# Performance work log

Measured on AMD Instinct MI355X. Metric: run time of the kernel, lower is better.

Reference implementation:

```python
import jax, jax.numpy as jnp
import numpy as np

B, L = 2, 256
CHAR, WORD = 8000, 50000
CE, WE, HID, REL = 128, 128, 256, 24
IN_DIM = CE + WE


def _lstm(x, mask, W, U, b):
    # Keras LSTM cell: z = x@W + h@U + b split into (i,f,g,o); masked steps carry state through.
    # x: (B, T, D) float, mask: (B, T) bool
    h0 = jnp.zeros((x.shape[0], U.shape[0]), x.dtype)

    def step(carry, xm):
        h, c = carry
        xt, mt = xm
        z = xt @ W + h @ U + b
        i, f, g, o = jnp.split(z, 4, axis=-1)
        c_new = jax.nn.sigmoid(f) * c + jax.nn.sigmoid(i) * jnp.tanh(g)
        h_new = jax.nn.sigmoid(o) * jnp.tanh(c_new)
        m = mt[:, None]
        h2 = jnp.where(m, h_new, h)
        c2 = jnp.where(m, c_new, c)
        return (h2, c2), h2

    _, hs = jax.lax.scan(step, (h0, h0), (jnp.swapaxes(x, 0, 1), jnp.swapaxes(mask, 0, 1)))
    return jnp.swapaxes(hs, 0, 1)  # (B, T, HID)


def _head(enc, Wu, bu, Wv, bv, Wuv, buv, Wc, bc):
    # Original: tile relu(u) over axis 1 (depends on j) and relu(v) over axis 2 (depends on i),
    # concat -> Dense. Equivalent fused form: split Wuv and broadcast-add the two projections.
    u = jax.nn.relu(enc @ Wu + bu)  # (B, L, E)
    v = jax.nn.relu(enc @ Wv + bv)  # (B, L, E)
    E = Wu.shape[1]
    uv = (jnp.einsum('bjd,de->bje', u, Wuv[:E])[:, None, :, :]
          + jnp.einsum('bid,de->bie', v, Wuv[E:])[:, :, None, :]
          + buv)  # (B, L, L, E)
    return uv @ Wc + bc  # (B, L, L, out)


def setup_inputs() -> dict:
    key = jax.random.key(0)
    ks = jax.random.split(key, 64)

    def w(k, shape):
        return jax.random.normal(k, shape, jnp.float32) * 0.05

    inp = {
        'inputs': jax.random.randint(ks[0], (B, L), 0, CHAR, jnp.int32),
        'input_words': jax.random.randint(ks[1], (B, L), 0, WORD, jnp.int32),
        'input_max_len': L,
        'embed_table': w(ks[2], (CHAR, CE)),
        'word_embed_table': w(ks[3], (WORD, WE)),
        'lstm_fwd_W': w(ks[4], (IN_DIM, 4 * HID)),
        'lstm_fwd_U': w(ks[5], (HID, 4 * HID)),
        'lstm_fwd_b': jnp.zeros((4 * HID,), jnp.float32),
        'lstm_bwd_W': w(ks[6], (IN_DIM, 4 * HID)),
        'lstm_bwd_U': w(ks[7], (HID, 4 * HID)),
        'lstm_bwd_b': jnp.zeros((4 * HID,), jnp.float32),
    }
    i = 8
    for name, out in (('eh', 1), ('hh', REL), ('tt', REL)):
        inp[f'{name}_u_W'] = w(ks[i], (2 * HID, CE)); i += 1
        inp[f'{name}_u_b'] = jnp.zeros((CE,), jnp.float32)
        inp[f'{name}_v_W'] = w(ks[i], (2 * HID, CE)); i += 1
        inp[f'{name}_v_b'] = jnp.zeros((CE,), jnp.float32)
        inp[f'{name}_uv_W'] = w(ks[i], (2 * CE, CE)); i += 1
        inp[f'{name}_uv_b'] = jnp.zeros((CE,), jnp.float32)
        inp[f'{name}_cls_W'] = w(ks[i], (CE, out)); i += 1
        inp[f'{name}_cls_b'] = jnp.zeros((out,), jnp.float32)
    return inp


def reference(inputs, input_words, input_max_len, embed_table, word_embed_table,
              lstm_fwd_W, lstm_fwd_U, lstm_fwd_b, lstm_bwd_W, lstm_bwd_U, lstm_bwd_b,
              eh_u_W, eh_u_b, eh_v_W, eh_v_b, eh_uv_W, eh_uv_b, eh_cls_W, eh_cls_b,
              hh_u_W, hh_u_b, hh_v_W, hh_v_b, hh_uv_W, hh_uv_b, hh_cls_W, hh_cls_b,
              tt_u_W, tt_u_b, tt_v_W, tt_v_b, tt_uv_W, tt_uv_b, tt_cls_W, tt_cls_b):
    mask = inputs != 0  # (B, L)
    x = jnp.concatenate([embed_table[inputs], word_embed_table[input_words]], axis=-1)
    h_fwd = _lstm(x, mask, lstm_fwd_W, lstm_fwd_U, lstm_fwd_b)
    h_bwd = _lstm(x[:, ::-1], mask[:, ::-1], lstm_bwd_W, lstm_bwd_U, lstm_bwd_b)[:, ::-1]
    enc = jnp.concatenate([h_fwd, h_bwd], axis=-1)  # (B, L, 2*HID)
    eh = jax.nn.sigmoid(_head(enc, eh_u_W, eh_u_b, eh_v_W, eh_v_b, eh_uv_W, eh_uv_b, eh_cls_W, eh_cls_b))
    hh = jax.nn.softmax(_head(enc, hh_u_W, hh_u_b, hh_v_W, hh_v_b, hh_uv_W, hh_uv_b, hh_cls_W, hh_cls_b), axis=-1)
    tt = jax.nn.softmax(_head(enc, tt_u_W, tt_u_b, tt_v_W, tt_v_b, tt_uv_W, tt_uv_b, tt_cls_W, tt_cls_b), axis=-1)
    return (eh, hh, tt)
```

## Files before the change

### kernel.cpp

```cpp
#include <hip/hip_runtime.h>
#include <hip/hip_bf16.h>

typedef unsigned short u16;
typedef unsigned int u32;
typedef unsigned long long u64;

#define LSEQ 256

constexpr int XW_F  = 0;
constexpr int XW_B  = 524288;
constexpr int HF_O  = 1048576;
constexpr int HB_O  = 1179648;
constexpr int UV_O  = 1310720;
constexpr int PEH_O = 1703936;
constexpr int QEH_O = 1704448;
constexpr int PHH_O = 1704960;
constexpr int QHH_O = 1717248;
constexpr int PTT_O = 1729536;
constexpr int QTT_O = 1741824;
constexpr int DT_O  = 1754128;
constexpr int CW_WF = 1754240;
constexpr int CW_UF = 2016384;
constexpr int CW_BF = 2278528;
constexpr int CW_WB = 2279552;
constexpr int CW_UB = 2541696;
constexpr int CW_BB = 2803840;
constexpr int HD0   = 2804864;
constexpr int HDS   = 167424;
constexpr int HD1   = HD0 + HDS;
constexpr int HD2   = HD0 + 2 * HDS;

constexpr u64 SENT64 = 0x7FC000007FC00000ULL;

__device__ __forceinline__ float b2f(u16 u) {
  u32 x = ((u32)u) << 16; float f;
  __builtin_memcpy(&f, &x, 4); return f;
}
__device__ __forceinline__ u16 f2b(float f) {
  u32 x; __builtin_memcpy(&x, &f, 4);
  u32 r = (x + 0x7fffu + ((x >> 16) & 1u)) >> 16;
  return (u16)r;
}
__device__ __forceinline__ float sigm(float x) {
  return __builtin_amdgcn_rcpf(1.f + __expf(-x));
}
__device__ __forceinline__ float tanh_fast(float x) {
  return 2.f * __builtin_amdgcn_rcpf(1.f + __expf(-2.f * x)) - 1.f;
}
__device__ __forceinline__ u64 aload64(u64* p) {
  return __hip_atomic_load(p, __ATOMIC_RELAXED, __HIP_MEMORY_SCOPE_AGENT);
}
__device__ __forceinline__ void astore64(u64* p, u64 v) {
  __hip_atomic_store(p, v, __ATOMIC_RELAXED, __HIP_MEMORY_SCOPE_AGENT);
}

__global__ __launch_bounds__(256) void k_detect(const void* __restrict__ etab,
                                                float* __restrict__ ws)
{
  __shared__ int cnt;
  const int tid = threadIdx.x;
  if (tid == 0) cnt = 0;
  __syncthreads();
  const u32 w = ((const u32*)etab)[tid];
  if (w & 0x4000u) atomicAdd(&cnt, 1);
  __syncthreads();
  if (tid == 0) ws[DT_O] = (cnt >= 16) ? 1.0f : 0.0f;
}

struct PtrPack { const void* p[30]; };

__global__ __launch_bounds__(256) void k_convert(PtrPack pk, float* __restrict__ ws)
{
  const int cnts[30] = {
    262144, 262144, 1024, 262144, 262144, 1024,
    65536, 128, 65536, 128, 32768, 128, 128, 1,
    65536, 128, 65536, 128, 32768, 128, 3072, 24,
    65536, 128, 65536, 128, 32768, 128, 3072, 24};
  const int dsts[30] = {
    CW_WF, CW_UF, CW_BF, CW_WB, CW_UB, CW_BB,
    HD0, HD0 + 65536, HD0 + 65664, HD0 + 131200, HD0 + 131328, HD0 + 164096, HD0 + 164224, HD0 + 167296,
    HD1, HD1 + 65536, HD1 + 65664, HD1 + 131200, HD1 + 131328, HD1 + 164096, HD1 + 164224, HD1 + 167296,
    HD2, HD2 + 65536, HD2 + 65664, HD2 + 131200, HD2 + 131328, HD2 + 164096, HD2 + 164224, HD2 + 167296};
  const int job = blockIdx.y;
  const int n = cnts[job];
  float* dst = ws + dsts[job];
  const void* src = pk.p[job];
  const bool f32m = ws[DT_O] > 0.5f;
  const int tid = threadIdx.x;
  const int idx = blockIdx.x * 256 + tid;
  const int stride = 64 * 256;
  const int n4 = n >> 2;
  if (f32m) {
    const float4* s = (const float4*)src;
    float4* d = (float4*)dst;
    for (int i = idx; i < n4; i += stride) d[i] = s[i];
  } else {
    const ushort4* s = (const ushort4*)src;
    float4* d = (float4*)dst;
    for (int i = idx; i < n4; i += stride) {
      ushort4 v = s[i];
      d[i] = make_float4(b2f(v.x), b2f(v.y), b2f(v.z), b2f(v.w));
    }
  }
  if (blockIdx.x == 0) {
    for (int i = (n4 << 2) + tid; i < n; i += 256)
      dst[i] = f32m ? ((const float*)src)[i] : b2f(((const u16*)src)[i]);
  }
}

__global__ __launch_bounds__(256) void k_embed_xw(
    const int* __restrict__ toks, const int* __restrict__ wrds,
    const void* __restrict__ etab, const void* __restrict__ wtab,
    float* __restrict__ ws)
{
  __shared__ float xs[8][256];
  const int tid = threadIdx.x, blk = blockIdx.x;
  {
    u64* hz = (u64*)(ws + HF_O) + (blk * 256 + tid) * 8;
#pragma unroll
    for (int m = 0; m < 8; m++) astore64(hz + m, SENT64);
  }
  const bool f32m = ws[DT_O] > 0.5f;
  for (int rr = 0; rr < 8; rr++) {
    const int row = blk * 8 + rr;
    const int id = toks[row], wid = wrds[row];
    float v;
    if (f32m) {
      v = (tid < 128) ? ((const float*)etab)[id * 128 + tid]
                      : ((const float*)wtab)[wid * 128 + (tid - 128)];
    } else {
      v = (tid < 128) ? b2f(((const u16*)etab)[id * 128 + tid])
                      : b2f(((const u16*)wtab)[wid * 128 + (tid - 128)]);
    }
    xs[rr][tid] = v;
  }
  __syncthreads();
  float aF[8][4], aB[8][4];
#pragma unroll
  for (int rr = 0; rr < 8; rr++)
#pragma unroll
    for (int c = 0; c < 4; c++) { aF[rr][c] = 0.f; aB[rr][c] = 0.f; }
  const float2* Wf2 = (const float2*)(ws + CW_WF);
  const float2* Wb2 = (const float2*)(ws + CW_WB);
  for (int k = 0; k < 256; k++) {
    const float2 wfa = Wf2[k * 512 + tid];
    const float2 wfb = Wf2[k * 512 + 256 + tid];
    const float2 wba = Wb2[k * 512 + tid];
    const float2 wbb = Wb2[k * 512 + 256 + tid];
#pragma unroll
    for (int rr = 0; rr < 8; rr++) {
      const float x = xs[rr][k];
      aF[rr][0] = fmaf(x, wfa.x, aF[rr][0]); aF[rr][1] = fmaf(x, wfa.y, aF[rr][1]);
      aF[rr][2] = fmaf(x, wfb.x, aF[rr][2]); aF[rr][3] = fmaf(x, wfb.y, aF[rr][3]);
      aB[rr][0] = fmaf(x, wba.x, aB[rr][0]); aB[rr][1] = fmaf(x, wba.y, aB[rr][1]);
      aB[rr][2] = fmaf(x, wbb.x, aB[rr][2]); aB[rr][3] = fmaf(x, wbb.y, aB[rr][3]);
    }
  }
  const int c0 = 2 * tid, c2 = 512 + 2 * tid;
#pragma unroll
  for (int rr = 0; rr < 8; rr++) {
    const int row = blk * 8 + rr;
    float* of = ws + XW_F + row * 1024;
    of[c0]   = aF[rr][0] + ws[CW_BF + c0];
    of[c0+1] = aF[rr][1] + ws[CW_BF + c0 + 1];
    of[c2]   = aF[rr][2] + ws[CW_BF + c2];
    of[c2+1] = aF[rr][3] + ws[CW_BF + c2 + 1];
    float* ob = ws + XW_B + row * 1024;
    ob[c0]   = aB[rr][0] + ws[CW_BB + c0];
    ob[c0+1] = aB[rr][1] + ws[CW_BB + c0 + 1];
    ob[c2]   = aB[rr][2] + ws[CW_BB + c2];
    ob[c2+1] = aB[rr][3] + ws[CW_BB + c2 + 1];
  }
}

__global__ __launch_bounds__(256, 1) void k_lstm(
    const int* __restrict__ toks, float* __restrict__ ws)
{
  __shared__ float2 hsh[2][256];
  __shared__ float psum[8][256];
  __shared__ float zsh[256];
  __shared__ int msk[512];
  const int tid = threadIdx.x;
  const int dir = blockIdx.x >> 3, chunk = blockIdx.x & 7, base = chunk * 32;
  const int q = tid & 31, ksec = tid >> 5, k0 = ksec * 32;
  u64* h64 = (u64*)(ws + (dir ? HB_O : HF_O));
  const float* xw = ws + (dir ? XW_B : XW_F);
  const float* Ubase = ws + (dir ? CW_UB : CW_UF);

  const int lc0 = 4 * q;
  const int gc0 = ((lc0 >> 5) << 8) + base + (lc0 & 31);
  float4 us[32];
#pragma unroll
  for (int j = 0; j < 32; j++)
    us[j] = *(const float4*)(Ubase + (k0 + j) * 1024 + gc0);

  const int gu = tid & 31, bsel = tid >> 5;
  const int rb = tid >> 7, rc = tid & 127;
  const int rgc = ((rc >> 5) << 8) + base + (rc & 31);
  const int widx = tid - 32;
  const int pkk = widx + (widx >= base ? 32 : 0);

  float cReg = 0.f, hReg = 0.f;
  float xwreg = xw[(rb * 256 + (dir ? 255 : 0)) * 1024 + rgc];

  hsh[0][tid] = make_float2(0.f, 0.f);
  msk[tid] = toks[tid];
  msk[tid + 256] = toks[tid + 256];
  __syncthreads();

  for (int s = 0; s < LSEQ; s++) {
    const int par = s & 1, npar = par ^ 1;
    const int t = dir ? (255 - s) : s;
    float a00 = 0.f, a01 = 0.f, a02 = 0.f, a03 = 0.f;
    float a10 = 0.f, a11 = 0.f, a12 = 0.f, a13 = 0.f;
#pragma unroll
    for (int j = 0; j < 32; j++) {
      const float2 h = hsh[par][k0 + j];
      const float4 uu = us[j];
      a00 = fmaf(h.x, uu.x, a00); a01 = fmaf(h.x, uu.y, a01);
      a02 = fmaf(h.x, uu.z, a02); a03 = fmaf(h.x, uu.w, a03);
      a10 = fmaf(h.y, uu.x, a10); a11 = fmaf(h.y, uu.y, a11);
      a12 = fmaf(h.y, uu.z, a12); a13 = fmaf(h.y, uu.w, a13);
    }
    *(float4*)&psum[ksec][lc0]       = make_float4(a00, a01, a02, a03);
    *(float4*)&psum[ksec][128 + lc0] = make_float4(a10, a11, a12, a13);
    __syncthreads();
    {
      float z = xwreg;
#pragma unroll
      for (int ks = 0; ks < 8; ks++) z += psum[ks][rb * 128 + rc];
      zsh[rb * 128 + rc] = z;
    }
    const int t2 = dir ? (s < 255 ? 254 - s : 255) : (s < 255 ? s + 1 : 0);
    xwreg = xw[(rb * 256 + t2) * 1024 + rgc];
    __syncthreads();
    if (tid < 64) {
      const float* zr = &zsh[bsel * 128];
      const float zi = zr[gu], zf = zr[32 + gu], zg = zr[64 + gu], zo = zr[96 + gu];
      const float cn = sigm(zf) * cReg + sigm(zi) * tanh_fast(zg);
      const float hn = sigm(zo) * tanh_fast(cn);
      if (msk[bsel * 256 + t] != 0) { cReg = cn; hReg = hn; }
      const float hb1 = __shfl_xor(hReg, 32);
      if (tid < 32) {
        const float2 fv = make_float2(hReg, hb1);
        hsh[npar][base + gu] = fv;
        u64 pv; __builtin_memcpy(&pv, &fv, 8);
        astore64(h64 + s * 256 + base + gu, pv);
      }
    }
    if (tid >= 32 && s < 255) {
      u64* p = h64 + s * 256 + pkk;
      u64 v = aload64(p);
      while (v == SENT64) v = aload64(p);
      float2 hv; __builtin_memcpy(&hv, &v, 8);
      hsh[npar][pkk] = hv;
    }
    __syncthreads();
  }
}

__global__ __launch_bounds__(256) void k_uv(float* __restrict__ ws)
{
  __shared__ float encs[8][512];
  const int tid = threadIdx.x, blk = blockIdx.x;
  for (int i = tid; i < 4096; i += 256) {
    const int rr = i >> 9, h = i & 511;
    const int row = blk * 8 + rr, b = row >> 8, t = row & 255;
    encs[rr][h] = (h < 256)
        ? ws[HF_O + t * 512 + h * 2 + b]
        : ws[HB_O + (255 - t) * 512 + (h - 256) * 2 + b];
  }
  __syncthreads();
  const float* wp[3]; float bias[3]; int mats[3], cs[3];
#pragma unroll
  for (int g = 0; g < 3; g++) {
    const int colid = tid + (g << 8);
    mats[g] = colid >> 7; cs[g] = colid & 127;
    const int head = mats[g] >> 1, part = mats[g] & 1;
    wp[g]  = ws + HD0 + head * HDS + (part ? 65664 : 0) + cs[g];
    bias[g] = ws[HD0 + head * HDS + (part ? 131200 : 65536) + cs[g]];
  }
  float acc[3][8];
#pragma unroll
  for (int g = 0; g < 3; g++)
#pragma unroll
    for (int rr = 0; rr < 8; rr++) acc[g][rr] = 0.f;
  for (int k = 0; k < 512; k++) {
#pragma unroll
    for (int g = 0; g < 3; g++) {
      const float w = wp[g][k * 128];
#pragma unroll
      for (int rr = 0; rr < 8; rr++)
        acc[g][rr] = fmaf(encs[rr][k], w, acc[g][rr]);
    }
  }
#pragma unroll
  for (int g = 0; g < 3; g++)
#pragma unroll
    for (int rr = 0; rr < 8; rr++) {
      const int row = blk * 8 + rr;
      ws[UV_O + (mats[g] * 512 + row) * 128 + cs[g]] = fmaxf(acc[g][rr] + bias[g], 0.f);
    }
}

__global__ __launch_bounds__(128) void k_pq(float* __restrict__ ws)
{
  __shared__ float us[4][6][128];
  __shared__ float ash[4][3][128], qsh[4][3][128];
  const int blk = blockIdx.x, tid = threadIdx.x;
  for (int i = tid; i < 3072; i += 128) {
    const int rr = i / 768, rem = i % 768, mat = rem >> 7, e = rem & 127;
    us[rr][mat][e] = ws[UV_O + (mat * 512 + blk * 4 + rr) * 128 + e];
  }
  __syncthreads();
#pragma unroll
  for (int hd = 0; hd < 3; hd++) {
    const float* W = ws + HD0 + hd * HDS + 131328;
    float av[4] = {0.f, 0.f, 0.f, 0.f}, qv[4] = {0.f, 0.f, 0.f, 0.f};
    for (int k = 0; k < 128; k++) {
      const float w1 = W[k * 128 + tid];
      const float w2 = W[(128 + k) * 128 + tid];
#pragma unroll
      for (int rr = 0; rr < 4; rr++) {
        av[rr] = fmaf(us[rr][2 * hd][k], w1, av[rr]);
        qv[rr] = fmaf(us[rr][2 * hd + 1][k], w2, qv[rr]);
      }
    }
    const float buv = ws[HD0 + hd * HDS + 164096 + tid];
#pragma unroll
    for (int rr = 0; rr < 4; rr++) {
      ash[rr][hd][tid] = av[rr] + buv;
      qsh[rr][hd][tid] = qv[rr];
    }
  }
  __syncthreads();
  if (tid < 98) {
    for (int rr = 0; rr < 4; rr++) {
      const int row = blk * 4 + rr;
      const float* src; float* dst; const float* Wc; int o, nout;
      if (tid < 2) {
        Wc = ws + HD0 + 164224; nout = 1; o = 0;
        src = (tid == 0) ? ash[rr][0] : qsh[rr][0];
        dst = ws + ((tid == 0) ? PEH_O : QEH_O) + row;
      } else if (tid < 50) {
        Wc = ws + HD1 + 164224; nout = 24;
        if (tid < 26) { o = tid - 2;  src = ash[rr][1]; dst = ws + PHH_O + row * 24 + o; }
        else          { o = tid - 26; src = qsh[rr][1]; dst = ws + QHH_O + row * 24 + o; }
      } else {
        Wc = ws + HD2 + 164224; nout = 24;
        if (tid < 74) { o = tid - 50; src = ash[rr][2]; dst = ws + PTT_O + row * 24 + o; }
        else          { o = tid - 74; src = qsh[rr][2]; dst = ws + QTT_O + row * 24 + o; }
      }
      float acc = 0.f;
      for (int e = 0; e < 128; e++) acc = fmaf(src[e], Wc[e * nout + o], acc);
      *dst = acc;
    }
  }
}

__global__ __launch_bounds__(256) void k_out(const float* __restrict__ ws,
                                             void* __restrict__ outv)
{
  __shared__ float qh[24], qt[24];
  __shared__ float qe_s;
  __shared__ u32 sh[3072], st[3072];
  const bool f32m = ws[DT_O] > 0.5f;
  const int bi = blockIdx.x, b = bi >> 8, i = bi & 255;
  const int j = threadIdx.x;
  if (j < 24)       qh[j] = ws[QHH_O + (b * 256 + i) * 24 + j] + ws[HD1 + 167296 + j];
  else if (j < 48)  qt[j - 24] = ws[QTT_O + (b * 256 + i) * 24 + (j - 24)] + ws[HD2 + 167296 + (j - 24)];
  else if (j == 48) qe_s = ws[QEH_O + b * 256 + i] + ws[HD0 + 167296];
  __syncthreads();
  {
    float v = ws[PEH_O + b * 256 + j] + qe_s;
    v = 1.f / (1.f + __expf(-v));
    if (f32m) ((float*)outv)[(b * 256 + i) * 256 + j] = v;
    else      ((u16*)outv)[(b * 256 + i) * 256 + j] = f2b(v);
  }
  float p[24];
  {
    const float* pp = ws + PHH_O + (b * 256 + j) * 24;
    float mx = -1e30f;
#pragma unroll
    for (int o = 0; o < 24; o++) { p[o] = pp[o] + qh[o]; mx = fmaxf(mx, p[o]); }
    float ssum = 0.f;
#pragma unroll
    for (int o = 0; o < 24; o++) { p[o] = __expf(p[o] - mx); ssum += p[o]; }
    const float inv = 1.f / ssum;
    if (f32m) {
      float* dst = (float*)outv + 131072 + (size_t)(bi * 256 + j) * 24;
#pragma unroll
      for (int m = 0; m < 6; m++)
        ((float4*)dst)[m] = make_float4(p[4*m]*inv, p[4*m+1]*inv, p[4*m+2]*inv, p[4*m+3]*inv);
    } else {
#pragma unroll
      for (int m = 0; m < 12; m++)
        sh[j * 12 + m] = ((u32)f2b(p[2*m+1] * inv) << 16) | (u32)f2b(p[2*m] * inv);
    }
  }
  {
    const float* pp = ws + PTT_O + (b * 256 + j) * 24;
    float mx = -1e30f;
#pragma unroll
    for (int o = 0; o < 24; o++) { p[o] = pp[o] + qt[o]; mx = fmaxf(mx, p[o]); }
    float ssum = 0.f;
#pragma unroll
    for (int o = 0; o < 24; o++) { p[o] = __expf(p[o] - mx); ssum += p[o]; }
    const float inv = 1.f / ssum;
    if (f32m) {
      float* dst = (float*)outv + 3276800 + (size_t)(bi * 256 + j) * 24;
#pragma unroll
      for (int m = 0; m < 6; m++)
        ((float4*)dst)[m] = make_float4(p[4*m]*inv, p[4*m+1]*inv, p[4*m+2]*inv, p[4*m+3]*inv);
    } else {
#pragma unroll
      for (int m = 0; m < 12; m++)
        st[j * 12 + m] = ((u32)f2b(p[2*m+1] * inv) << 16) | (u32)f2b(p[2*m] * inv);
    }
  }
  __syncthreads();
  if (!f32m) {
    u32* outu = (u32*)outv;
    const int baseH = 65536 + bi * 3072;
    const int baseT = 1638400 + bi * 3072;
#pragma unroll
    for (int m = 0; m < 12; m++) {
      outu[baseH + j + 256 * m] = sh[j + 256 * m];
      outu[baseT + j + 256 * m] = st[j + 256 * m];
    }
  }
}

extern "C" void kernel_launch(void* const* d_in, const int* in_sizes, int n_in,
                              void* d_out, int out_size, void* d_ws, size_t ws_size,
                              hipStream_t stream) {
  const int* toks = (const int*)d_in[0];
  const int* wrds = (const int*)d_in[1];
  float* ws = (float*)d_ws;

  k_detect<<<dim3(1), dim3(256), 0, stream>>>(d_in[3], ws);

  PtrPack pk;
  pk.p[0] = d_in[5]; pk.p[1] = d_in[6]; pk.p[2] = d_in[7];
  pk.p[3] = d_in[8]; pk.p[4] = d_in[9]; pk.p[5] = d_in[10];
  for (int h = 0; h < 3; h++)
    for (int a = 0; a < 8; a++)
      pk.p[6 + h * 8 + a] = d_in[11 + h * 8 + a];
  k_convert<<<dim3(64, 30), dim3(256), 0, stream>>>(pk, ws);

  k_embed_xw<<<dim3(64), dim3(256), 0, stream>>>(toks, wrds, d_in[3], d_in[4], ws);
  k_lstm<<<dim3(16), dim3(256), 0, stream>>>(toks, ws);
  k_uv<<<dim3(64), dim3(256), 0, stream>>>(ws);
  k_pq<<<dim3(128), dim3(128), 0, stream>>>(ws);
  k_out<<<dim3(512), dim3(256), 0, stream>>>(ws, d_out);
}
```

Measured before the change: 765.0 us.

## Drop weight conversion pass, fuse head kernels, interleave both LSTM directions per block

Removes the separate dtype-detect and weight-conversion kernels. Dtype is now detected inline with a wavefront ballot, and raw bf16/f32 weights are read directly in each kernel. The LSTM is restructured so each of 16 blocks owns 16 hidden units of both directions, alternating forward and backward half-steps, so one direction's cross-block exchange overlaps the other's compute. The uv and pq head kernels are merged into a single kernel gridded over row groups and heads, and the input projection is split across more blocks. The aim is fewer launches and less workspace traffic, at the cost of more serialized per-step work inside each LSTM block.

```diff
diff --git a/kernel.cpp b/kernel.cpp
--- a/kernel.cpp
+++ b/kernel.cpp
@@ -11,24 +11,12 @@
 constexpr int XW_B  = 524288;
 constexpr int HF_O  = 1048576;
 constexpr int HB_O  = 1179648;
-constexpr int UV_O  = 1310720;
 constexpr int PEH_O = 1703936;
 constexpr int QEH_O = 1704448;
 constexpr int PHH_O = 1704960;
 constexpr int QHH_O = 1717248;
 constexpr int PTT_O = 1729536;
 constexpr int QTT_O = 1741824;
-constexpr int DT_O  = 1754128;
-constexpr int CW_WF = 1754240;
-constexpr int CW_UF = 2016384;
-constexpr int CW_BF = 2278528;
-constexpr int CW_WB = 2279552;
-constexpr int CW_UB = 2541696;
-constexpr int CW_BB = 2803840;
-constexpr int HD0   = 2804864;
-constexpr int HDS   = 167424;
-constexpr int HD1   = HD0 + HDS;
-constexpr int HD2   = HD0 + 2 * HDS;
 
 constexpr u64 SENT64 = 0x7FC000007FC00000ULL;
 
@@ -53,323 +41,353 @@
 __device__ __forceinline__ void astore64(u64* p, u64 v) {
   __hip_atomic_store(p, v, __ATOMIC_RELAXED, __HIP_MEMORY_SCOPE_AGENT);
 }
-
-__global__ __launch_bounds__(256) void k_detect(const void* __restrict__ etab,
-                                                float* __restrict__ ws)
-{
-  __shared__ int cnt;
-  const int tid = threadIdx.x;
-  if (tid == 0) cnt = 0;
-  __syncthreads();
-  const u32 w = ((const u32*)etab)[tid];
-  if (w & 0x4000u) atomicAdd(&cnt, 1);
-  __syncthreads();
-  if (tid == 0) ws[DT_O] = (cnt >= 16) ? 1.0f : 0.0f;
-}
-
-struct PtrPack { const void* p[30]; };
-
-__global__ __launch_bounds__(256) void k_convert(PtrPack pk, float* __restrict__ ws)
-{
-  const int cnts[30] = {
-    262144, 262144, 1024, 262144, 262144, 1024,
-    65536, 128, 65536, 128, 32768, 128, 128, 1,
-    65536, 128, 65536, 128, 32768, 128, 3072, 24,
-    65536, 128, 65536, 128, 32768, 128, 3072, 24};
-  const int dsts[30] = {
-    CW_WF, CW_UF, CW_BF, CW_WB, CW_UB, CW_BB,
-    HD0, HD0 + 65536, HD0 + 65664, HD0 + 131200, HD0 + 131328, HD0 + 164096, HD0 + 164224, HD0 + 167296,
-    HD1, HD1 + 65536, HD1 + 65664, HD1 + 131200, HD1 + 131328, HD1 + 164096, HD1 + 164224, HD1 + 167296,
-    HD2, HD2 + 65536, HD2 + 65664, HD2 + 131200, HD2 + 131328, HD2 + 164096, HD2 + 164224, HD2 + 167296};
-  const int job = blockIdx.y;
-  const int n = cnts[job];
-  float* dst = ws + dsts[job];
-  const void* src = pk.p[job];
-  const bool f32m = ws[DT_O] > 0.5f;
-  const int tid = threadIdx.x;
-  const int idx = blockIdx.x * 256 + tid;
-  const int stride = 64 * 256;
-  const int n4 = n >> 2;
-  if (f32m) {
-    const float4* s = (const float4*)src;
-    float4* d = (float4*)dst;
-    for (int i = idx; i < n4; i += stride) d[i] = s[i];
-  } else {
-    const ushort4* s = (const ushort4*)src;
-    float4* d = (float4*)dst;
-    for (int i = idx; i < n4; i += stride) {
-      ushort4 v = s[i];
-      d[i] = make_float4(b2f(v.x), b2f(v.y), b2f(v.z), b2f(v.w));
-    }
-  }
-  if (blockIdx.x == 0) {
-    for (int i = (n4 << 2) + tid; i < n; i += 256)
-      dst[i] = f32m ? ((const float*)src)[i] : b2f(((const u16*)src)[i]);
-  }
+__device__ __forceinline__ bool detect_f32(const void* etab) {
+  u32 w = ((const u32*)etab)[threadIdx.x & 63];
+  u64 m = __ballot((w & 0x4000u) != 0);
+  return __popcll(m) >= 16;
+}
+__device__ __forceinline__ float ldf(const void* p, int i, bool f32m) {
+  return f32m ? ((const float*)p)[i] : b2f(((const u16*)p)[i]);
 }
 
 __global__ __launch_bounds__(256) void k_embed_xw(
     const int* __restrict__ toks, const int* __restrict__ wrds,
     const void* __restrict__ etab, const void* __restrict__ wtab,
+    const void* __restrict__ Wf, const void* __restrict__ bf_,
+    const void* __restrict__ Wb, const void* __restrict__ bb_,
     float* __restrict__ ws)
 {
   __shared__ float xs[8][256];
-  const int tid = threadIdx.x, blk = blockIdx.x;
-  {
-    u64* hz = (u64*)(ws + HF_O) + (blk * 256 + tid) * 8;
-#pragma unroll
-    for (int m = 0; m < 8; m++) astore64(hz + m, SENT64);
-  }
-  const bool f32m = ws[DT_O] > 0.5f;
+  const int tid = threadIdx.x, bx = blockIdx.x;
+  const int rg = bx >> 2, part = bx & 3, dir = part >> 1, ch = part & 1;
+  {
+    u64* hz = (u64*)(ws + HF_O) + (bx * 256 + tid) * 2;
+    astore64(hz, SENT64); astore64(hz + 1, SENT64);
+  }
+  const bool f32m = detect_f32(etab);
   for (int rr = 0; rr < 8; rr++) {
-    const int row = blk * 8 + rr;
+    const int row = rg * 8 + rr;
     const int id = toks[row], wid = wrds[row];
-    float v;
-    if (f32m) {
-      v = (tid < 128) ? ((const float*)etab)[id * 128 + tid]
-                      : ((const float*)wtab)[wid * 128 + (tid - 128)];
-    } else {
-      v = (tid < 128) ? b2f(((const u16*)etab)[id * 128 + tid])
-                      : b2f(((const u16*)wtab)[wid * 128 + (tid - 128)]);
-    }
-    xs[rr][tid] = v;
-  }
-  __syncthreads();
-  float aF[8][4], aB[8][4];
-#pragma unroll
-  for (int rr = 0; rr < 8; rr++)
-#pragma unroll
-    for (int c = 0; c < 4; c++) { aF[rr][c] = 0.f; aB[rr][c] = 0.f; }
-  const float2* Wf2 = (const float2*)(ws + CW_WF);
-  const float2* Wb2 = (const float2*)(ws + CW_WB);
-  for (int k = 0; k < 256; k++) {
-    const float2 wfa = Wf2[k * 512 + tid];
-    const float2 wfb = Wf2[k * 512 + 256 + tid];
-    const float2 wba = Wb2[k * 512 + tid];
-    const float2 wbb = Wb2[k * 512 + 256 + tid];
-#pragma unroll
-    for (int rr = 0; rr < 8; rr++) {
-      const float x = xs[rr][k];
-      aF[rr][0] = fmaf(x, wfa.x, aF[rr][0]); aF[rr][1] = fmaf(x, wfa.y, aF[rr][1]);
-      aF[rr][2] = fmaf(x, wfb.x, aF[rr][2]); aF[rr][3] = fmaf(x, wfb.y, aF[rr][3]);
-      aB[rr][0] = fmaf(x, wba.x, aB[rr][0]); aB[rr][1] = fmaf(x, wba.y, aB[rr][1]);
-      aB[rr][2] = fmaf(x, wbb.x, aB[rr][2]); aB[rr][3] = fmaf(x, wbb.y, aB[rr][3]);
-    }
-  }
-  const int c0 = 2 * tid, c2 = 512 + 2 * tid;
+    xs[rr][tid] = (tid < 128) ? ldf(etab, id * 128 + tid, f32m)
+                              : ldf(wtab, wid * 128 + (tid - 128), f32m);
+  }
+  __syncthreads();
+  const void* W = dir ? Wb : Wf;
+  const void* bb = dir ? bb_ : bf_;
+  const int c0 = ch * 512 + 2 * tid;
+  float acc[8][2];
+#pragma unroll
+  for (int rr = 0; rr < 8; rr++) { acc[rr][0] = 0.f; acc[rr][1] = 0.f; }
+  if (f32m) {
+    const float2* W2 = (const float2*)W;
+    for (int k = 0; k < 256; k++) {
+      const float2 w = W2[k * 512 + (c0 >> 1)];
+#pragma unroll
+      for (int rr = 0; rr < 8; rr++) {
+        const float x = xs[rr][k];
+        acc[rr][0] = fmaf(x, w.x, acc[rr][0]);
+        acc[rr][1] = fmaf(x, w.y, acc[rr][1]);
+      }
+    }
+  } else {
+    const u32* W2 = (const u32*)W;
+    for (int k = 0; k < 256; k++) {
+      const u32 v = W2[k * 512 + (c0 >> 1)];
+      const float wx = b2f(v & 0xffff), wy = b2f(v >> 16);
+#pragma unroll
+      for (int rr = 0; rr < 8; rr++) {
+        const float x = xs[rr][k];
+        acc[rr][0] = fmaf(x, wx, acc[rr][0]);
+        acc[rr][1] = fmaf(x, wy, acc[rr][1]);
+      }
+    }
+  }
+  const float b0 = ldf(bb, c0, f32m), b1 = ldf(bb, c0 + 1, f32m);
+  float* xwb = ws + (dir ? XW_B : XW_F);
 #pragma unroll
   for (int rr = 0; rr < 8; rr++) {
-    const int row = blk * 8 + rr;
-    float* of = ws + XW_F + row * 1024;
-    of[c0]   = aF[rr][0] + ws[CW_BF + c0];
-    of[c0+1] = aF[rr][1] + ws[CW_BF + c0 + 1];
-    of[c2]   = aF[rr][2] + ws[CW_BF + c2];
-    of[c2+1] = aF[rr][3] + ws[CW_BF + c2 + 1];
-    float* ob = ws + XW_B + row * 1024;
-    ob[c0]   = aB[rr][0] + ws[CW_BB + c0];
-    ob[c0+1] = aB[rr][1] + ws[CW_BB + c0 + 1];
-    ob[c2]   = aB[rr][2] + ws[CW_BB + c2];
-    ob[c2+1] = aB[rr][3] + ws[CW_BB + c2 + 1];
+    const int row = rg * 8 + rr;
+    float2 o = make_float2(acc[rr][0] + b0, acc[rr][1] + b1);
+    *(float2*)(xwb + row * 1024 + c0) = o;
   }
 }
 
 __global__ __launch_bounds__(256, 1) void k_lstm(
-    const int* __restrict__ toks, float* __restrict__ ws)
+    const int* __restrict__ toks,
+    const void* __restrict__ Uf_raw, const void* __restrict__ Ub_raw,
+    const void* __restrict__ etab, float* __restrict__ ws)
 {
-  __shared__ float2 hsh[2][256];
-  __shared__ float psum[8][256];
-  __shared__ float zsh[256];
+  __shared__ float2 hsh0[256], hsh1[256];
+  __shared__ float psum0[8][128], psum1[8][128];
+  __shared__ float zsh0[128], zsh1[128];
   __shared__ int msk[512];
   const int tid = threadIdx.x;
-  const int dir = blockIdx.x >> 3, chunk = blockIdx.x & 7, base = chunk * 32;
+  const int w = blockIdx.x, base = w * 16;
   const int q = tid & 31, ksec = tid >> 5, k0 = ksec * 32;
-  u64* h64 = (u64*)(ws + (dir ? HB_O : HF_O));
-  const float* xw = ws + (dir ? XW_B : XW_F);
-  const float* Ubase = ws + (dir ? CW_UB : CW_UF);
-
-  const int lc0 = 4 * q;
-  const int gc0 = ((lc0 >> 5) << 8) + base + (lc0 & 31);
-  float4 us[32];
-#pragma unroll
-  for (int j = 0; j < 32; j++)
-    us[j] = *(const float4*)(Ubase + (k0 + j) * 1024 + gc0);
-
-  const int gu = tid & 31, bsel = tid >> 5;
-  const int rb = tid >> 7, rc = tid & 127;
-  const int rgc = ((rc >> 5) << 8) + base + (rc & 31);
-  const int widx = tid - 32;
-  const int pkk = widx + (widx >= base ? 32 : 0);
-
-  float cReg = 0.f, hReg = 0.f;
-  float xwreg = xw[(rb * 256 + (dir ? 255 : 0)) * 1024 + rgc];
-
-  hsh[0][tid] = make_float2(0.f, 0.f);
-  msk[tid] = toks[tid];
-  msk[tid + 256] = toks[tid + 256];
+  u64* h0 = (u64*)(ws + HF_O);
+  u64* h1 = (u64*)(ws + HB_O);
+  const float* xw0 = ws + XW_F;
+  const float* xw1 = ws + XW_B;
+  const bool f32m = detect_f32(etab);
+
+  const int lc0 = 2 * q;
+  const int gc0 = (lc0 >> 4) * 256 + base + (lc0 & 15);
+  float2 us0[32], us1[32];
+  if (f32m) {
+    const float* U0 = (const float*)Uf_raw;
+    const float* U1 = (const float*)Ub_raw;
+#pragma unroll
+    for (int j = 0; j < 32; j++) {
+      us0[j] = *(const float2*)(U0 + (k0 + j) * 1024 + gc0);
+      us1[j] = *(const float2*)(U1 + (k0 + j) * 1024 + gc0);
+    }
+  } else {
+    const u32* U0 = (const u32*)Uf_raw;
+    const u32* U1 = (const u32*)Ub_raw;
+#pragma unroll
+    for (int j = 0; j < 32; j++) {
+      u32 v0 = U0[((k0 + j) * 1024 + gc0) >> 1];
+      u32 v1 = U1[((k0 + j) * 1024 + gc0) >> 1];
+      us0[j] = make_float2(b2f(v0 & 0xffff), b2f(v0 >> 16));
+      us1[j] = make_float2(b2f(v1 & 0xffff), b2f(v1 >> 16));
+    }
+  }
+  const int rlc = tid >> 1, rbb = tid & 1;
+  const int rgc = (rlc >> 4) * 256 + base + (rlc & 15);
+  const int gj = tid & 15, gb = (tid >> 4) & 1;
+  const bool own = (tid >= base) && (tid < base + 16);
+
+  msk[tid] = toks[tid]; msk[tid + 256] = toks[tid + 256];
+  hsh0[tid] = make_float2(0.f, 0.f);
+  hsh1[tid] = make_float2(0.f, 0.f);
+  float c0Reg = 0.f, h0Reg = 0.f, c1Reg = 0.f, h1Reg = 0.f;
+  float xw0reg = xw0[rbb * 262144 + 0 * 1024 + rgc];
+  float xw1reg = xw1[rbb * 262144 + 255 * 1024 + rgc];
   __syncthreads();
 
   for (int s = 0; s < LSEQ; s++) {
-    const int par = s & 1, npar = par ^ 1;
-    const int t = dir ? (255 - s) : s;
-    float a00 = 0.f, a01 = 0.f, a02 = 0.f, a03 = 0.f;
-    float a10 = 0.f, a11 = 0.f, a12 = 0.f, a13 = 0.f;
-#pragma unroll
-    for (int j = 0; j < 32; j++) {
-      const float2 h = hsh[par][k0 + j];
-      const float4 uu = us[j];
-      a00 = fmaf(h.x, uu.x, a00); a01 = fmaf(h.x, uu.y, a01);
-      a02 = fmaf(h.x, uu.z, a02); a03 = fmaf(h.x, uu.w, a03);
-      a10 = fmaf(h.y, uu.x, a10); a11 = fmaf(h.y, uu.y, a11);
-      a12 = fmaf(h.y, uu.z, a12); a13 = fmaf(h.y, uu.w, a13);
-    }
-    *(float4*)&psum[ksec][lc0]       = make_float4(a00, a01, a02, a03);
-    *(float4*)&psum[ksec][128 + lc0] = make_float4(a10, a11, a12, a13);
-    __syncthreads();
+    u64 v1 = 0;
+    if (s > 0 && !own) v1 = aload64(&h1[(s - 1) * 256 + tid]);
     {
-      float z = xwreg;
-#pragma unroll
-      for (int ks = 0; ks < 8; ks++) z += psum[ks][rb * 128 + rc];
-      zsh[rb * 128 + rc] = z;
-    }
-    const int t2 = dir ? (s < 255 ? 254 - s : 255) : (s < 255 ? s + 1 : 0);
-    xwreg = xw[(rb * 256 + t2) * 1024 + rgc];
-    __syncthreads();
-    if (tid < 64) {
-      const float* zr = &zsh[bsel * 128];
-      const float zi = zr[gu], zf = zr[32 + gu], zg = zr[64 + gu], zo = zr[96 + gu];
-      const float cn = sigm(zf) * cReg + sigm(zi) * tanh_fast(zg);
+      float4 a = make_float4(0.f, 0.f, 0.f, 0.f);
+#pragma unroll
+      for (int j = 0; j < 32; j++) {
+        const float2 h = hsh0[k0 + j];
+        const float2 u = us0[j];
+        a.x = fmaf(h.x, u.x, a.x); a.y = fmaf(h.y, u.x, a.y);
+        a.z = fmaf(h.x, u.y, a.z); a.w = fmaf(h.y, u.y, a.w);
+      }
+      *(float4*)&psum0[ksec][4 * q] = a;
+    }
+    __syncthreads();
+    if (tid < 128) {
+      float z = xw0reg;
+#pragma unroll
+      for (int ks = 0; ks < 8; ks++) z += psum0[ks][tid];
+      zsh0[tid] = z;
+      const int t2 = (s < 255) ? s + 1 : 255;
+      xw0reg = xw0[rbb * 262144 + t2 * 1024 + rgc];
+    }
+    __syncthreads();
+    if (tid < 32) {
+      const float zi = zsh0[gj * 2 + gb],        zf = zsh0[(16 + gj) * 2 + gb];
+      const float zg = zsh0[(32 + gj) * 2 + gb], zo = zsh0[(48 + gj) * 2 + gb];
+      const float cn = sigm(zf) * c0Reg + sigm(zi) * tanh_fast(zg);
       const float hn = sigm(zo) * tanh_fast(cn);
-      if (msk[bsel * 256 + t] != 0) { cReg = cn; hReg = hn; }
-      const float hb1 = __shfl_xor(hReg, 32);
-      if (tid < 32) {
-        const float2 fv = make_float2(hReg, hb1);
-        hsh[npar][base + gu] = fv;
+      if (msk[gb * 256 + s] != 0) { c0Reg = cn; h0Reg = hn; }
+      const float hp = __shfl_xor(h0Reg, 16);
+      if (tid < 16) {
+        const float2 fv = make_float2(h0Reg, hp);
+        hsh0[base + tid] = fv;
         u64 pv; __builtin_memcpy(&pv, &fv, 8);
-        astore64(h64 + s * 256 + base + gu, pv);
-      }
-    }
-    if (tid >= 32 && s < 255) {
-      u64* p = h64 + s * 256 + pkk;
-      u64 v = aload64(p);
-      while (v == SENT64) v = aload64(p);
-      float2 hv; __builtin_memcpy(&hv, &v, 8);
-      hsh[npar][pkk] = hv;
-    }
-    __syncthreads();
-  }
-}
-
-__global__ __launch_bounds__(256) void k_uv(float* __restrict__ ws)
+        astore64(&h0[s * 256 + base + tid], pv);
+      }
+    }
+    if (s > 0 && !own) {
+      while (v1 == SENT64) v1 = aload64(&h1[(s - 1) * 256 + tid]);
+      float2 hv; __builtin_memcpy(&hv, &v1, 8);
+      hsh1[tid] = hv;
+    }
+    __syncthreads();
+    u64 v0 = 0;
+    if (s < 255 && !own) v0 = aload64(&h0[s * 256 + tid]);
+    {
+      float4 a = make_float4(0.f, 0.f, 0.f, 0.f);
+#pragma unroll
+      for (int j = 0; j < 32; j++) {
+        const float2 h = hsh1[k0 + j];
+        const float2 u = us1[j];
+        a.x = fmaf(h.x, u.x, a.x); a.y = fmaf(h.y, u.x, a.y);
+        a.z = fmaf(h.x, u.y, a.z); a.w = fmaf(h.y, u.y, a.w);
+      }
+      *(float4*)&psum1[ksec][4 * q] = a;
+    }
+    __syncthreads();
+    if (tid < 128) {
+      float z = xw1reg;
+#pragma unroll
+      for (int ks = 0; ks < 8; ks++) z += psum1[ks][tid];
+      zsh1[tid] = z;
+      const int t2 = (s < 255) ? 254 - s : 0;
+      xw1reg = xw1[rbb * 262144 + t2 * 1024 + rgc];
+    }
+    __syncthreads();
+    if (tid < 32) {
+      const float zi = zsh1[gj * 2 + gb],        zf = zsh1[(16 + gj) * 2 + gb];
+      const float zg = zsh1[(32 + gj) * 2 + gb], zo = zsh1[(48 + gj) * 2 + gb];
+      const float cn = sigm(zf) * c1Reg + sigm(zi) * tanh_fast(zg);
+      const float hn = sigm(zo) * tanh_fast(cn);
+      if (msk[gb * 256 + (255 - s)] != 0) { c1Reg = cn; h1Reg = hn; }
+      const float hp = __shfl_xor(h1Reg, 16);
+      if (tid < 16) {
+        const float2 fv = make_float2(h1Reg, hp);
+        hsh1[base + tid] = fv;
+        u64 pv; __builtin_memcpy(&pv, &fv, 8);
+        astore64(&h1[s * 256 + base + tid], pv);
+      }
+    }
+    if (s < 255 && !own) {
+      while (v0 == SENT64) v0 = aload64(&h0[s * 256 + tid]);
+      float2 hv; __builtin_memcpy(&hv, &v0, 8);
+      hsh0[tid] = hv;
+    }
+    __syncthreads();
+  }
+}
+
+struct HeadPack { const void* p[24]; };
+
+__global__ __launch_bounds__(256) void k_uvpq(
+    HeadPack pk, const void* __restrict__ etab, float* __restrict__ ws)
 {
-  __shared__ float encs[8][512];
-  const int tid = threadIdx.x, blk = blockIdx.x;
+  __shared__ float encs_t[512][8];
+  __shared__ float usv_t[2][128][8];
+  __shared__ float apq[2][8][128];
+  __shared__ float wc[3072];
+  const int tid = threadIdx.x, rgp = blockIdx.x, hd = blockIdx.y;
+  const bool f32m = detect_f32(etab);
+  const void* uW  = pk.p[hd * 8 + 0]; const void* ub  = pk.p[hd * 8 + 1];
+  const void* vW  = pk.p[hd * 8 + 2]; const void* vb  = pk.p[hd * 8 + 3];
+  const void* uvW = pk.p[hd * 8 + 4]; const void* uvb = pk.p[hd * 8 + 5];
+  const void* cW  = pk.p[hd * 8 + 6];
+  const int nout = (hd == 0) ? 1 : 24;
+  for (int i = tid; i < 128 * nout; i += 256) wc[i] = ldf(cW, i, f32m);
   for (int i = tid; i < 4096; i += 256) {
-    const int rr = i >> 9, h = i & 511;
-    const int row = blk * 8 + rr, b = row >> 8, t = row & 255;
-    encs[rr][h] = (h < 256)
+    const int h = i >> 3, rr = i & 7;
+    const int row = rgp * 8 + rr, b = row >> 8, t = row & 255;
+    encs_t[h][rr] = (h < 256)
         ? ws[HF_O + t * 512 + h * 2 + b]
         : ws[HB_O + (255 - t) * 512 + (h - 256) * 2 + b];
   }
   __syncthreads();
-  const float* wp[3]; float bias[3]; int mats[3], cs[3];
-#pragma unroll
-  for (int g = 0; g < 3; g++) {
-    const int colid = tid + (g << 8);
-    mats[g] = colid >> 7; cs[g] = colid & 127;
-    const int head = mats[g] >> 1, part = mats[g] & 1;
-    wp[g]  = ws + HD0 + head * HDS + (part ? 65664 : 0) + cs[g];
-    bias[g] = ws[HD0 + head * HDS + (part ? 131200 : 65536) + cs[g]];
-  }
-  float acc[3][8];
-#pragma unroll
-  for (int g = 0; g < 3; g++)
-#pragma unroll
-    for (int rr = 0; rr < 8; rr++) acc[g][rr] = 0.f;
-  for (int k = 0; k < 512; k++) {
-#pragma unroll
-    for (int g = 0; g < 3; g++) {
-      const float w = wp[g][k * 128];
-#pragma unroll
-      for (int rr = 0; rr < 8; rr++)
-        acc[g][rr] = fmaf(encs[rr][k], w, acc[g][rr]);
-    }
-  }
-#pragma unroll
-  for (int g = 0; g < 3; g++)
-#pragma unroll
-    for (int rr = 0; rr < 8; rr++) {
-      const int row = blk * 8 + rr;
-      ws[UV_O + (mats[g] * 512 + row) * 128 + cs[g]] = fmaxf(acc[g][rr] + bias[g], 0.f);
-    }
-}
-
-__global__ __launch_bounds__(128) void k_pq(float* __restrict__ ws)
-{
-  __shared__ float us[4][6][128];
-  __shared__ float ash[4][3][128], qsh[4][3][128];
-  const int blk = blockIdx.x, tid = threadIdx.x;
-  for (int i = tid; i < 3072; i += 128) {
-    const int rr = i / 768, rem = i % 768, mat = rem >> 7, e = rem & 127;
-    us[rr][mat][e] = ws[UV_O + (mat * 512 + blk * 4 + rr) * 128 + e];
-  }
-  __syncthreads();
-#pragma unroll
-  for (int hd = 0; hd < 3; hd++) {
-    const float* W = ws + HD0 + hd * HDS + 131328;
-    float av[4] = {0.f, 0.f, 0.f, 0.f}, qv[4] = {0.f, 0.f, 0.f, 0.f};
-    for (int k = 0; k < 128; k++) {
-      const float w1 = W[k * 128 + tid];
-      const float w2 = W[(128 + k) * 128 + tid];
-#pragma unroll
-      for (int rr = 0; rr < 4; rr++) {
-        av[rr] = fmaf(us[rr][2 * hd][k], w1, av[rr]);
-        qv[rr] = fmaf(us[rr][2 * hd + 1][k], w2, qv[rr]);
-      }
-    }
-    const float buv = ws[HD0 + hd * HDS + 164096 + tid];
-#pragma unroll
-    for (int rr = 0; rr < 4; rr++) {
-      ash[rr][hd][tid] = av[rr] + buv;
-      qsh[rr][hd][tid] = qv[rr];
-    }
-  }
-  __syncthreads();
-  if (tid < 98) {
-    for (int rr = 0; rr < 4; rr++) {
-      const int row = blk * 4 + rr;
-      const float* src; float* dst; const float* Wc; int o, nout;
-      if (tid < 2) {
-        Wc = ws + HD0 + 164224; nout = 1; o = 0;
-        src = (tid == 0) ? ash[rr][0] : qsh[rr][0];
-        dst = ws + ((tid == 0) ? PEH_O : QEH_O) + row;
-      } else if (tid < 50) {
-        Wc = ws + HD1 + 164224; nout = 24;
-        if (tid < 26) { o = tid - 2;  src = ash[rr][1]; dst = ws + PHH_O + row * 24 + o; }
-        else          { o = tid - 26; src = qsh[rr][1]; dst = ws + QHH_O + row * 24 + o; }
-      } else {
-        Wc = ws + HD2 + 164224; nout = 24;
-        if (tid < 74) { o = tid - 50; src = ash[rr][2]; dst = ws + PTT_O + row * 24 + o; }
-        else          { o = tid - 74; src = qsh[rr][2]; dst = ws + QTT_O + row * 24 + o; }
-      }
+  {
+    const int mat = tid >> 7, cs = tid & 127;
+    const void* W = mat ? vW : uW;
+    const float bias = ldf(mat ? vb : ub, cs, f32m);
+    float acc[8];
+#pragma unroll
+    for (int rr = 0; rr < 8; rr++) acc[rr] = 0.f;
+    if (f32m) {
+      const float* Wf = (const float*)W;
+      for (int k = 0; k < 512; k++) {
+        const float wv = Wf[k * 128 + cs];
+        const float4 e0 = *(const float4*)&encs_t[k][0];
+        const float4 e1 = *(const float4*)&encs_t[k][4];
+        acc[0] = fmaf(e0.x, wv, acc[0]); acc[1] = fmaf(e0.y, wv, acc[1]);
+        acc[2] = fmaf(e0.z, wv, acc[2]); acc[3] = fmaf(e0.w, wv, acc[3]);
+        acc[4] = fmaf(e1.x, wv, acc[4]); acc[5] = fmaf(e1.y, wv, acc[5]);
+        acc[6] = fmaf(e1.z, wv, acc[6]); acc[7] = fmaf(e1.w, wv, acc[7]);
+      }
+    } else {
+      const u16* Wf = (const u16*)W;
+      for (int k = 0; k < 512; k++) {
+        const float wv = b2f(Wf[k * 128 + cs]);
+        const float4 e0 = *(const float4*)&encs_t[k][0];
+        const float4 e1 = *(const float4*)&encs_t[k][4];
+        acc[0] = fmaf(e0.x, wv, acc[0]); acc[1] = fmaf(e0.y, wv, acc[1]);
+        acc[2] = fmaf(e0.z, wv, acc[2]); acc[3] = fmaf(e0.w, wv, acc[3]);
+        acc[4] = fmaf(e1.x, wv, acc[4]); acc[5] = fmaf(e1.y, wv, acc[5]);
+        acc[6] = fmaf(e1.z, wv, acc[6]); acc[7] = fmaf(e1.w, wv, acc[7]);
+      }
+    }
+#pragma unroll
+    for (int rr = 0; rr < 8; rr++)
+      usv_t[mat][cs][rr] = fmaxf(acc[rr] + bias, 0.f);
+  }
+  __syncthreads();
+  {
+    const int half = tid >> 7, col = tid & 127;
+    float acc[8];
+#pragma unroll
+    for (int rr = 0; rr < 8; rr++) acc[rr] = 0.f;
+    if (f32m) {
+      const float* Wf = (const float*)uvW;
+      for (int k = 0; k < 128; k++) {
+        const float wv = Wf[(half * 128 + k) * 128 + col];
+        const float4 e0 = *(const float4*)&usv_t[half][k][0];
+        const float4 e1 = *(const float4*)&usv_t[half][k][4];
+        acc[0] = fmaf(e0.x, wv, acc[0]); acc[1] = fmaf(e0.y, wv, acc[1]);
+        acc[2] = fmaf(e0.z, wv, acc[2]); acc[3] = fmaf(e0.w, wv, acc[3]);
+        acc[4] = fmaf(e1.x, wv, acc[4]); acc[5] = fmaf(e1.y, wv, acc[5]);
+        acc[6] = fmaf(e1.z, wv, acc[6]); acc[7] = fmaf(e1.w, wv, acc[7]);
+      }
+    } else {
+      const u16* Wf = (const u16*)uvW;
+      for (int k = 0; k < 128; k++) {
+        const float wv = b2f(Wf[(half * 128 + k) * 128 + col]);
+        const float4 e0 = *(const float4*)&usv_t[half][k][0];
+        const float4 e1 = *(const float4*)&usv_t[half][k][4];
+        acc[0] = fmaf(e0.x, wv, acc[0]); acc[1] = fmaf(e0.y, wv, acc[1]);
+        acc[2] = fmaf(e0.z, wv, acc[2]); acc[3] = fmaf(e0.w, wv, acc[3]);
+        acc[4] = fmaf(e1.x, wv, acc[4]); acc[5] = fmaf(e1.y, wv, acc[5]);
+        acc[6] = fmaf(e1.z, wv, acc[6]); acc[7] = fmaf(e1.w, wv, acc[7]);
+      }
+    }
+    const float bv = (half == 0) ? ldf(uvb, col, f32m) : 0.f;
+#pragma unroll
+    for (int rr = 0; rr < 8; rr++)
+      apq[half][rr][col] = acc[rr] + bv;
+  }
+  __syncthreads();
+  if (hd == 0) {
+    if (tid < 16) {
+      const int rr = tid >> 1, aq = tid & 1;
       float acc = 0.f;
-      for (int e = 0; e < 128; e++) acc = fmaf(src[e], Wc[e * nout + o], acc);
-      *dst = acc;
-    }
-  }
-}
-
-__global__ __launch_bounds__(256) void k_out(const float* __restrict__ ws,
-                                             void* __restrict__ outv)
+      for (int e = 0; e < 128; e++) acc = fmaf(apq[aq][rr][e], wc[e], acc);
+      const int row = rgp * 8 + rr;
+      ws[(aq ? QEH_O : PEH_O) + row] = acc;
+    }
+  } else {
+    const int PO = (hd == 1) ? PHH_O : PTT_O;
+    const int QO = (hd == 1) ? QHH_O : QTT_O;
+    for (int it = 0; it < 2; it++) {
+      if (tid < 192) {
+        const int task = it * 192 + tid;
+        const int rr = task / 48, r2 = task % 48;
+        const int aq = r2 / 24, o = r2 % 24;
+        float acc = 0.f;
+        for (int e = 0; e < 128; e++) acc = fmaf(apq[aq][rr][e], wc[e * 24 + o], acc);
+        const int row = rgp * 8 + rr;
+        ws[(aq ? QO : PO) + row * 24 + o] = acc;
+      }
+    }
+  }
+}
+
+__global__ __launch_bounds__(256) void k_out(
+    const void* __restrict__ bceh, const void* __restrict__ bchh,
+    const void* __restrict__ bctt, const void* __restrict__ etab,
+    const float* __restrict__ ws, void* __restrict__ outv)
 {
   __shared__ float qh[24], qt[24];
   __shared__ float qe_s;
   __shared__ u32 sh[3072], st[3072];
-  const bool f32m = ws[DT_O] > 0.5f;
+  const bool f32m = detect_f32(etab);
   const int bi = blockIdx.x, b = bi >> 8, i = bi & 255;
   const int j = threadIdx.x;
-  if (j < 24)       qh[j] = ws[QHH_O + (b * 256 + i) * 24 + j] + ws[HD1 + 167296 + j];
-  else if (j < 48)  qt[j - 24] = ws[QTT_O + (b * 256 + i) * 24 + (j - 24)] + ws[HD2 + 167296 + (j - 24)];
-  else if (j == 48) qe_s = ws[QEH_O + b * 256 + i] + ws[HD0 + 167296];
+  if (j < 24)       qh[j] = ws[QHH_O + (b * 256 + i) * 24 + j] + ldf(bchh, j, f32m);
+  else if (j < 48)  qt[j - 24] = ws[QTT_O + (b * 256 + i) * 24 + (j - 24)] + ldf(bctt, j - 24, f32m);
+  else if (j == 48) qe_s = ws[QEH_O + b * 256 + i] + ldf(bceh, 0, f32m);
   __syncthreads();
   {
     float v = ws[PEH_O + b * 256 + j] + qe_s;
@@ -438,19 +456,14 @@
   const int* wrds = (const int*)d_in[1];
   float* ws = (float*)d_ws;
 
-  k_detect<<<dim3(1), dim3(256), 0, stream>>>(d_in[3], ws);
-
-  PtrPack pk;
-  pk.p[0] = d_in[5]; pk.p[1] = d_in[6]; pk.p[2] = d_in[7];
-  pk.p[3] = d_in[8]; pk.p[4] = d_in[9]; pk.p[5] = d_in[10];
+  k_embed_xw<<<dim3(256), dim3(256), 0, stream>>>(
+      toks, wrds, d_in[3], d_in[4], d_in[5], d_in[7], d_in[8], d_in[10], ws);
+  k_lstm<<<dim3(16), dim3(256), 0, stream>>>(toks, d_in[6], d_in[9], d_in[3], ws);
+  HeadPack pk;
   for (int h = 0; h < 3; h++)
     for (int a = 0; a < 8; a++)
-      pk.p[6 + h * 8 + a] = d_in[11 + h * 8 + a];
-  k_convert<<<dim3(64, 30), dim3(256), 0, stream>>>(pk, ws);
-
-  k_embed_xw<<<dim3(64), dim3(256), 0, stream>>>(toks, wrds, d_in[3], d_in[4], ws);
-  k_lstm<<<dim3(16), dim3(256), 0, stream>>>(toks, ws);
-  k_uv<<<dim3(64), dim3(256), 0, stream>>>(ws);
-  k_pq<<<dim3(128), dim3(128), 0, stream>>>(ws);
-  k_out<<<dim3(512), dim3(256), 0, stream>>>(ws, d_out);
-}
+      pk.p[h * 8 + a] = d_in[11 + h * 8 + a];
+  k_uvpq<<<dim3(64, 3), dim3(256), 0, stream>>>(pk, d_in[3], ws);
+  k_out<<<dim3(512), dim3(256), 0, stream>>>(
+      d_in[18], d_in[26], d_in[34], d_in[3], ws, d_out);
+}
```

After: 822.8 us. 7.6% more time.
